# Kernel optimization log

Hardware: AMD Instinct MI355X
Metric: run time of the kernel (lower is better)

The kernel has to match this reference:

```python
import jax, jax.numpy as jnp
import numpy as np

NUM_CLASSES = 22
SKIP = 20            # skip_pixels: stride over flattened pixel index
N_STEPS = 200        # discretized steps along each voting ray
STEP = 4.0           # pixels per ray step
INLIER_T = 0.9       # inlier_threshold on direction dot-product
LABEL_T = 500.0      # label_threshold: min #pixels of a class to be valid


def _hough_forward(label_2d, vertex_pred, extents, poses, meta_data):
    B, H, W = label_2d.shape
    C = NUM_CLASSES
    HW = H * W

    # ---- strided pixel sampling (skip_pixels) ----
    idx = jnp.arange(0, HW, SKIP)                      # [P]
    P = idx.shape[0]
    ys = (idx // W).astype(jnp.float32)                # [P]
    xs = (idx % W).astype(jnp.float32)
    labels = label_2d.reshape(B, HW)[:, idx].astype(jnp.int32)   # [B,P]
    vp = vertex_pred.reshape(B, HW, C, 3)[:, idx]                # [B,P,C,3]
    # pick each pixel's predicted (dx,dy,z) for its own class label
    sel = jnp.take_along_axis(
        vp, jnp.broadcast_to(labels[:, :, None, None], (B, P, 1, 3)), axis=2
    )[:, :, 0]                                                   # [B,P,3]
    d = sel[..., :2]
    dn = d / (jnp.linalg.norm(d, axis=-1, keepdims=True) + 1e-9)  # unit dir [B,P,2]
    z = sel[..., 2]                                               # [B,P]
    fg = labels > 0                                               # foreground mask

    # ---- ray voting into per-class Hough accumulator ----
    t = (jnp.arange(N_STEPS, dtype=jnp.float32) + 1.0) * STEP     # [T]
    cx = xs[None, :, None] + dn[..., 0:1] * t[None, None, :]      # [B,P,T]
    cy = ys[None, :, None] + dn[..., 1:2] * t[None, None, :]
    cxi = jnp.round(cx).astype(jnp.int32)
    cyi = jnp.round(cy).astype(jnp.int32)
    inb = (cxi >= 0) & (cxi < W) & (cyi >= 0) & (cyi < H) & fg[..., None]
    cxi = jnp.clip(cxi, 0, W - 1)
    cyi = jnp.clip(cyi, 0, H - 1)
    bidx = jnp.arange(B, dtype=jnp.int32)[:, None, None]
    flat = ((bidx * C + labels[:, :, None]) * H + cyi) * W + cxi  # [B,P,T]
    hough = jnp.zeros((B * C * HW,), jnp.float32)
    hough = hough.at[flat.reshape(-1)].add(inb.reshape(-1).astype(jnp.float32))
    hough = hough.reshape(B, C, H, W)

    # ---- per-class peak ----
    hflat = hough.reshape(B, C, HW)
    vmax = hflat.max(-1)                               # [B,C]
    pk = jnp.argmax(hflat, axis=-1).astype(jnp.int32)  # [B,C]
    pky = (pk // W).astype(jnp.float32)
    pkx = (pk % W).astype(jnp.float32)

    # ---- validity: enough labeled pixels for the class ----
    b2 = jnp.arange(B, dtype=jnp.int32)[:, None]
    counts = jnp.zeros((B, C), jnp.float32).at[
        jnp.broadcast_to(b2, (B, HW)).reshape(-1),
        label_2d.reshape(-1).astype(jnp.int32),
    ].add(1.0)                                          # [B,C] full-res pixel counts
    cls_ids = jnp.arange(C, dtype=jnp.float32)
    valid = (counts >= LABEL_T) & (cls_ids[None, :] > 0)  # [B,C]

    # ---- inlier selection + inlier-averaged depth ----
    cx_c = jnp.take_along_axis(pkx, labels, axis=1)    # [B,P] peak of pixel's class
    cy_c = jnp.take_along_axis(pky, labels, axis=1)
    dvec = jnp.stack([cx_c - xs[None, :], cy_c - ys[None, :]], axis=-1)
    dvec = dvec / (jnp.linalg.norm(dvec, axis=-1, keepdims=True) + 1e-9)
    dot = jnp.sum(dn * dvec, axis=-1)                  # [B,P]
    inl = (fg & (dot > INLIER_T)).astype(jnp.float32)  # [B,P]
    bP = jnp.broadcast_to(b2, (B, P)).reshape(-1)
    z_sum = jnp.zeros((B, C), jnp.float32).at[bP, labels.reshape(-1)].add((z * inl).reshape(-1))
    n_inl = jnp.zeros((B, C), jnp.float32).at[bP, labels.reshape(-1)].add(inl.reshape(-1))
    depth = z_sum / jnp.maximum(n_inl, 1.0)            # [B,C]
    z_safe = jnp.where(jnp.abs(depth) > 1e-3, depth, 1.0)

    # ---- bbox from extents + intrinsics ----
    fx = meta_data[:, 0:1]                             # [B,1]
    fy = meta_data[:, 4:5]
    diam = jnp.linalg.norm(extents, axis=-1)[None, :]  # [1,C]
    half_w = 0.5 * diam * fx / z_safe
    half_h = 0.5 * diam * fy / z_safe
    vmask = valid.astype(jnp.float32)
    rois = jnp.stack([
        jnp.broadcast_to(b2.astype(jnp.float32), (B, C)),
        jnp.broadcast_to(cls_ids[None, :], (B, C)),
        pkx - half_w, pky - half_h, pkx + half_w, pky + half_h,
        vmax,
    ], axis=-1) * vmask[..., None]                     # [B,C,7]

    # ---- pose init: identity quaternion + backprojected translation ----
    Kinv = meta_data[:, 9:18].reshape(B, 3, 3)
    hom = jnp.stack([pkx, pky, jnp.ones_like(pkx)], axis=-1)      # [B,C,3]
    ray = jnp.einsum('bij,bcj->bci', Kinv, hom)
    T = depth[..., None] * ray                                    # [B,C,3]
    quat = jnp.broadcast_to(jnp.array([1.0, 0.0, 0.0, 0.0], jnp.float32), (B, C, 4))
    pose_out = jnp.concatenate([quat, T], axis=-1) * vmask[..., None]  # [B,C,7]

    return jnp.concatenate([rois, pose_out], axis=-1)  # [B,C,14]


def setup_inputs() -> dict:
    key = jax.random.key(0)
    k1, k2, k3 = jax.random.split(key, 3)
    B, H, W = 2, 480, 640
    label_2d = jax.random.randint(k1, (B, H, W), 0, NUM_CLASSES, dtype=jnp.int32)
    vertex_pred = jax.random.normal(k2, (B, H, W, 3 * NUM_CLASSES), dtype=jnp.float32)
    extents = jax.random.uniform(k3, (NUM_CLASSES, 3), minval=0.05, maxval=0.3, dtype=jnp.float32)
    poses = jnp.zeros((B, 13), jnp.float32)
    K = np.array([[1066.778, 0, 312.9869], [0, 1067.487, 241.3109], [0, 0, 1]], dtype=np.float32)
    Kinv = np.linalg.pinv(K).astype(np.float32)
    md = np.zeros((B, 48), np.float32)
    md[:, 0:9] = K.flatten()
    md[:, 9:18] = Kinv.flatten()
    meta_data = jnp.asarray(md)
    return {"label_2d": label_2d, "vertex_pred": vertex_pred, "extents": extents,
            "poses": poses, "meta_data": meta_data}


def reference(label_2d, vertex_pred, extents, poses, meta_data):
    return _hough_forward(label_2d, vertex_pred, extents, poses, meta_data)
```

## Files before the change

kernel.cpp:

```cpp
#include <hip/hip_runtime.h>
#include <math.h>

#define C_      22
#define SKIP_   20
#define NSTEP_  200
#define STEP_   4.0f
#define INL_T_  0.9f
#define LAB_T_  500
#define B_      2
#define H_      480
#define W_      640
#define HW_     (H_ * W_)
#define P_      (HW_ / SKIP_)
#define NPTS_   (B_ * P_)

#define TS_       64
#define TILES_X_  (W_ / TS_)
#define NTILES_Y_ 8
#define NTILES_   (TILES_X_ * NTILES_Y_)
#define NPLANES_  (B_ * (C_ - 1))
#define NPT_      (NPLANES_ * NTILES_)

#define CMP_BLOCKS_   (NPTS_ / 256)
#define HIST_BLOCKS_  ((B_ * HW_) / (256 * 4))

#define KEY_INIT_ 0x00000000FFFFFFFFull

__global__ __launch_bounds__(256) void compact_hist_kernel(const int* __restrict__ label,
                                                           const float* __restrict__ vp,
                                                           unsigned int* __restrict__ cls_cnt,
                                                           uint4* __restrict__ cls,
                                                           int* __restrict__ counts,
                                                           unsigned long long* __restrict__ key) {
    const int tid = threadIdx.x;
    if (blockIdx.x < CMP_BLOCKS_) {
        __shared__ int hcnt[NPLANES_];
        __shared__ int hbase[NPLANES_];
        for (int i = tid; i < NPLANES_; i += 256) hcnt[i] = 0;
        __syncthreads();
        int g   = blockIdx.x * 256 + tid;
        int b   = g / P_;
        int pi  = g - b * P_;
        int idx = pi * SKIP_;
        int lab = label[b * HW_ + idx];
        int p = -1, slot = 0;
        uint4 r;
        if (lab > 0) {
            int xi = idx % W_, yi = idx / W_;
            const float* s = vp + ((size_t)(b * HW_ + idx) * (C_ * 3)) + lab * 3;
            float dx = s[0], dy = s[1], z = s[2];
            float nrm = sqrtf(__fadd_rn(__fmul_rn(dx, dx), __fmul_rn(dy, dy))) + 1e-9f;
            float dnx = dx / nrm, dny = dy / nrm;
            p = b * (C_ - 1) + (lab - 1);
            r.x = (unsigned)xi | ((unsigned)yi << 16);
            r.y = __float_as_uint(z);
            r.z = __float_as_uint(dnx);
            r.w = __float_as_uint(dny);
            slot = atomicAdd(&hcnt[p], 1);
        }
        __syncthreads();
        for (int i = tid; i < NPLANES_; i += 256) {
            int v = hcnt[i];
            hbase[i] = v ? (int)atomicAdd(&cls_cnt[i], (unsigned)v) : 0;
        }
        __syncthreads();
        if (p >= 0)
            cls[(size_t)p * P_ + hbase[p] + slot] = r;
    } else {
        __shared__ int h[C_];
        int cb  = blockIdx.x - CMP_BLOCKS_;
        if (cb == 0 && tid < B_ * C_)
            key[tid] = KEY_INIT_;
        const int bpb = HW_ / 1024;
        int b   = cb / bpb;
        int off = (cb % bpb) * 1024 + tid * 4;
        if (tid < C_) h[tid] = 0;
        __syncthreads();
        int4 l4 = *(const int4*)(label + b * HW_ + off);
        atomicAdd(&h[l4.x], 1);
        atomicAdd(&h[l4.y], 1);
        atomicAdd(&h[l4.z], 1);
        atomicAdd(&h[l4.w], 1);
        __syncthreads();
        if (tid < C_) {
            int v = h[tid];
            if (v) atomicAdd(&counts[b * C_ + tid], v);
        }
    }
}

__global__ __launch_bounds__(256) void raster_argmax_kernel(const uint4* __restrict__ cls,
                                                            const unsigned int* __restrict__ cls_cnt,
                                                            unsigned long long* __restrict__ key) {
    __shared__ unsigned int tile[TS_ * TS_ / 2];
    __shared__ unsigned int sv[4];
    __shared__ int          si[4];
    const int tid = threadIdx.x;
    int pt = blockIdx.x;
    int p  = pt / NTILES_;
    int tl = pt % NTILES_;
    int b = p / (C_ - 1);
    int c = p % (C_ - 1) + 1;
    int x0 = (tl % TILES_X_) * TS_;
    int y0 = (tl / TILES_X_) * TS_;
    {
        uint4* t4 = (uint4*)tile;
        t4[tid]       = make_uint4(0u, 0u, 0u, 0u);
        t4[tid + 256] = make_uint4(0u, 0u, 0u, 0u);
    }
    __syncthreads();

    int m = (int)cls_cnt[p];
    if (m > P_) m = P_;
    const uint4* cl = cls + (size_t)p * P_;
    const float lox = (float)x0 - 0.51f, hix = (float)x0 + 63.51f;
    const float loy = (float)y0 - 0.51f, hiy = (float)y0 + 63.51f;
    for (int rI = tid; rI < m; rI += 256) {
        uint4 rec = cl[rI];
        float xs  = (float)(rec.x & 0xFFFFu);
        float ys  = (float)(rec.x >> 16);
        float dnx = __uint_as_float(rec.z);
        float dny = __uint_as_float(rec.w);
        float tLo = STEP_, tHi = (float)NSTEP_ * STEP_;
        bool empty = false;
        if (fabsf(dnx) > 1e-8f) {
            float ta = (lox - xs) / dnx, tb = (hix - xs) / dnx;
            float t1 = fminf(ta, tb), t2 = fmaxf(ta, tb);
            tLo = fmaxf(tLo, t1); tHi = fminf(tHi, t2);
        } else if (xs < lox || xs > hix) { empty = true; }
        if (fabsf(dny) > 1e-8f) {
            float ta = (loy - ys) / dny, tb = (hiy - ys) / dny;
            float t1 = fminf(ta, tb), t2 = fmaxf(ta, tb);
            tLo = fmaxf(tLo, t1); tHi = fminf(tHi, t2);
        } else if (ys < loy || ys > hiy) { empty = true; }
        if (empty || tLo > tHi) continue;
        int iB = (int)floorf(tLo * 0.25f) - 2; if (iB < 0) iB = 0;
        int iE = (int)ceilf(tHi * 0.25f) + 2;  if (iE > NSTEP_ - 1) iE = NSTEP_ - 1;
        for (int i = iB; i <= iE; ++i) {
            float t = (float)(i + 1) * STEP_;
            float cx = __fadd_rn(xs, __fmul_rn(dnx, t));
            float cy = __fadd_rn(ys, __fmul_rn(dny, t));
            float cxr = rintf(cx);
            float cyr = rintf(cy);
            if (cxr >= 0.0f && cxr <= (float)(W_ - 1) && cyr >= 0.0f && cyr <= (float)(H_ - 1)) {
                int lx = (int)cxr - x0;
                int ly = (int)cyr - y0;
                if ((unsigned)lx < TS_ && (unsigned)ly < TS_) {
                    int cell = ly * TS_ + lx;
                    atomicAdd(&tile[cell >> 1], 1u << ((cell & 1) * 16));
                }
            }
        }
    }
    __syncthreads();
    unsigned bv = 0u; int bi = 0;
    {
        unsigned w0 = tile[tid];
        bv = w0 & 0xFFFFu; bi = tid * 2;
        unsigned hi = w0 >> 16;
        if (hi > bv) { bv = hi; bi = tid * 2 + 1; }
    }
    #pragma unroll
    for (int j = 1; j < 8; ++j) {
        int ix = tid + j * 256;
        unsigned w = tile[ix];
        unsigned lo = w & 0xFFFFu, hi = w >> 16;
        if (lo > bv) { bv = lo; bi = ix * 2; }
        if (hi > bv) { bv = hi; bi = ix * 2 + 1; }
    }
    #pragma unroll
    for (int s = 1; s < 64; s <<= 1) {
        unsigned ov = (unsigned)__shfl_xor((int)bv, s);
        int      oi = __shfl_xor(bi, s);
        if (ov > bv || (ov == bv && oi < bi)) { bv = ov; bi = oi; }
    }
    if ((tid & 63) == 0) { sv[tid >> 6] = bv; si[tid >> 6] = bi; }
    __syncthreads();
    if (tid == 0) {
        unsigned fbv = sv[0]; int fbi = si[0];
        #pragma unroll
        for (int w = 1; w < 4; ++w) {
            unsigned ov = sv[w]; int oi = si[w];
            if (ov > fbv || (ov == fbv && oi < fbi)) { fbv = ov; fbi = oi; }
        }
        if (fbv > 0u) {
            int ly = fbi >> 6, lx = fbi & 63;
            unsigned gidx = (unsigned)((y0 + ly) * W_ + (x0 + lx));
            unsigned long long k = ((unsigned long long)fbv << 32)
                                 | (unsigned long long)(0xFFFFFFFFu - gidx);
            atomicMax(&key[b * C_ + c], k);
        }
    }
}

__global__ __launch_bounds__(256) void inlier_finalize_kernel(const uint4* __restrict__ cls,
                                                              const unsigned int* __restrict__ cls_cnt,
                                                              const unsigned long long* __restrict__ key,
                                                              float* __restrict__ z_sum,
                                                              float* __restrict__ n_inl,
                                                              int* __restrict__ counts,
                                                              const float* __restrict__ extents,
                                                              const float* __restrict__ meta,
                                                              unsigned int* __restrict__ done,
                                                              float* __restrict__ out) {
    __shared__ float zp[4];
    __shared__ float np[4];
    __shared__ int last_flag;
    const int tid = threadIdx.x;
    int p = blockIdx.x;
    int b = p / (C_ - 1);
    int c = p % (C_ - 1) + 1;
    int t_ = b * C_ + c;
    unsigned long long kp = key[t_];
    int pkv = (int)(0xFFFFFFFFu - (unsigned int)(kp & 0xFFFFFFFFull));
    float pkx = (float)(pkv % W_), pky = (float)(pkv / W_);
    int m = (int)cls_cnt[p];
    if (m > P_) m = P_;
    const uint4* cl = cls + (size_t)p * P_;
    float zacc = 0.0f, nacc = 0.0f;
    for (int r = tid; r < m; r += 256) {
        uint4 rec = cl[r];
        float xs  = (float)(rec.x & 0xFFFFu);
        float ys  = (float)(rec.x >> 16);
        float z   = __uint_as_float(rec.y);
        float dnx = __uint_as_float(rec.z);
        float dny = __uint_as_float(rec.w);
        float dvx = __fsub_rn(pkx, xs), dvy = __fsub_rn(pky, ys);
        float nrm2 = sqrtf(__fadd_rn(__fmul_rn(dvx, dvx), __fmul_rn(dvy, dvy))) + 1e-9f;
        dvx /= nrm2; dvy /= nrm2;
        float dot = __fadd_rn(__fmul_rn(dnx, dvx), __fmul_rn(dny, dvy));
        if (dot > INL_T_) { zacc += z; nacc += 1.0f; }
    }
    #pragma unroll
    for (int s = 1; s < 64; s <<= 1) {
        zacc += __shfl_xor(zacc, s);
        nacc += __shfl_xor(nacc, s);
    }
    if ((tid & 63) == 0) { zp[tid >> 6] = zacc; np[tid >> 6] = nacc; }
    __syncthreads();
    if (tid == 0) {
        z_sum[t_] = zp[0] + zp[1] + zp[2] + zp[3];
        n_inl[t_] = np[0] + np[1] + np[2] + np[3];
        __threadfence();
        unsigned prev = atomicAdd(done, 1u);
        last_flag = (prev == (unsigned)(NPLANES_ - 1)) ? 1 : 0;
    }
    __syncthreads();
    if (!last_flag) return;
    __threadfence();
    int t = tid;
    if (t >= B_ * C_) return;
    int bb = t / C_, c2 = t % C_;
    float* o = out + t * 14;
    int   cnt_t  = atomicAdd(&counts[t], 0);
    bool valid = (cnt_t >= LAB_T_) && (c2 > 0);
    if (!valid) {
        #pragma unroll
        for (int k2 = 0; k2 < 14; ++k2) o[k2] = 0.0f;
        return;
    }
    float zsum_t = atomicAdd(&z_sum[t], 0.0f);
    float ninl_t = atomicAdd(&n_inl[t], 0.0f);
    unsigned long long k = atomicAdd((unsigned long long*)&key[0] + t, 0ull);
    float depth = zsum_t / fmaxf(ninl_t, 1.0f);
    float z_safe = (fabsf(depth) > 0.001f) ? depth : 1.0f;
    float fx = meta[bb * 48 + 0];
    float fy = meta[bb * 48 + 4];
    const float* e = extents + c2 * 3;
    float diam = sqrtf(e[0]*e[0] + e[1]*e[1] + e[2]*e[2]);
    float vmax = (float)(unsigned int)(k >> 32);
    int pkv2 = (int)(0xFFFFFFFFu - (unsigned int)(k & 0xFFFFFFFFull));
    float pkx2 = (float)(pkv2 % W_), pky2 = (float)(pkv2 / W_);
    float half_w = ((0.5f * diam) * fx) / z_safe;
    float half_h = ((0.5f * diam) * fy) / z_safe;
    o[0] = (float)bb;
    o[1] = (float)c2;
    o[2] = pkx2 - half_w;
    o[3] = pky2 - half_h;
    o[4] = pkx2 + half_w;
    o[5] = pky2 + half_h;
    o[6] = vmax;
    const float* Ki = meta + bb * 48 + 9;
    float rx = Ki[0]*pkx2 + Ki[1]*pky2 + Ki[2];
    float ry = Ki[3]*pkx2 + Ki[4]*pky2 + Ki[5];
    float rz = Ki[6]*pkx2 + Ki[7]*pky2 + Ki[8];
    o[7]  = 1.0f;
    o[8]  = 0.0f;
    o[9]  = 0.0f;
    o[10] = 0.0f;
    o[11] = depth * rx;
    o[12] = depth * ry;
    o[13] = depth * rz;
}

extern "C" void kernel_launch(void* const* d_in, const int* in_sizes, int n_in,
                              void* d_out, int out_size, void* d_ws, size_t ws_size,
                              hipStream_t stream) {
    const int*   label   = (const int*)d_in[0];
    const float* vp      = (const float*)d_in[1];
    const float* extents = (const float*)d_in[2];
    const float* meta    = (const float*)d_in[4];
    float* out = (float*)d_out;

    char* ws = (char*)d_ws;
    size_t off = 0;
    unsigned int* cls_cnt = (unsigned int*)(ws + off); off += NPLANES_ * sizeof(unsigned int);
    int*          counts  = (int*)(ws + off);          off += B_ * C_ * sizeof(int);
    unsigned int* done    = (unsigned int*)(ws + off); off += sizeof(unsigned int);
    size_t zero_bytes = off;
    off = (off + 15) & ~(size_t)15;
    float* z_sum  = (float*)(ws + off); off += B_ * C_ * sizeof(float);
    float* n_inl  = (float*)(ws + off); off += B_ * C_ * sizeof(float);
    off = (off + 15) & ~(size_t)15;
    unsigned long long* key = (unsigned long long*)(ws + off);
    off += B_ * C_ * sizeof(unsigned long long);
    off = (off + 15) & ~(size_t)15;
    uint4* cls = (uint4*)(ws + off);
    off += (size_t)NPLANES_ * P_ * sizeof(uint4);

    hipMemsetAsync(d_ws, 0, zero_bytes, stream);

    compact_hist_kernel<<<CMP_BLOCKS_ + HIST_BLOCKS_, 256, 0, stream>>>(
        label, vp, cls_cnt, cls, counts, key);
    raster_argmax_kernel<<<NPT_, 256, 0, stream>>>(cls, cls_cnt, key);
    inlier_finalize_kernel<<<NPLANES_, 256, 0, stream>>>(
        cls, cls_cnt, key, z_sum, n_inl, counts, extents, meta, done, out);
}
```

Baseline: 257.6 us.

## Fuse finalize into raster kernel, use per-block directory instead of global atomics

The pipeline drops from a memset plus three launches to two kernels. The first kernel now writes records block-locally, sorted by class through an LDS prefix scan. It saves a per-block directory of start and count for each class and per-block label histogram partials, so it needs no global atomics. The raster kernel rebuilds each plane's record list by scanning the directory and binary-searching per record. The last tile block of each plane then runs the inlier reduction and writes the output, which adds scan and search overhead to every tile block.

```diff
diff --git a/kernel.cpp b/kernel.cpp
--- a/kernel.cpp
+++ b/kernel.cpp
@@ -21,80 +21,106 @@
 #define NPLANES_  (B_ * (C_ - 1))
 #define NPT_      (NPLANES_ * NTILES_)
 
-#define CMP_BLOCKS_   (NPTS_ / 256)
-#define HIST_BLOCKS_  ((B_ * HW_) / (256 * 4))
+#define K1_BLOCKS_   (NPTS_ / 256)
+#define SLAB_        (B_ * HW_ / K1_BLOCKS_)
+#define HB_PER_IMG_  (K1_BLOCKS_ / B_)
 
 #define KEY_INIT_ 0x00000000FFFFFFFFull
 
 __global__ __launch_bounds__(256) void compact_hist_kernel(const int* __restrict__ label,
                                                            const float* __restrict__ vp,
-                                                           unsigned int* __restrict__ cls_cnt,
                                                            uint4* __restrict__ cls,
-                                                           int* __restrict__ counts,
-                                                           unsigned long long* __restrict__ key) {
+                                                           unsigned int* __restrict__ dir,
+                                                           unsigned int* __restrict__ partials,
+                                                           unsigned int* __restrict__ pdone,
+                                                           unsigned long long* __restrict__ key,
+                                                           float* __restrict__ out) {
+    __shared__ int   hcnt[NPLANES_];
+    __shared__ int   hstart[NPLANES_];
+    __shared__ uint4 stage[256];
+    __shared__ int   hh[C_];
     const int tid = threadIdx.x;
-    if (blockIdx.x < CMP_BLOCKS_) {
-        __shared__ int hcnt[NPLANES_];
-        __shared__ int hbase[NPLANES_];
-        for (int i = tid; i < NPLANES_; i += 256) hcnt[i] = 0;
-        __syncthreads();
-        int g   = blockIdx.x * 256 + tid;
-        int b   = g / P_;
-        int pi  = g - b * P_;
-        int idx = pi * SKIP_;
-        int lab = label[b * HW_ + idx];
-        int p = -1, slot = 0;
-        uint4 r;
-        if (lab > 0) {
-            int xi = idx % W_, yi = idx / W_;
-            const float* s = vp + ((size_t)(b * HW_ + idx) * (C_ * 3)) + lab * 3;
-            float dx = s[0], dy = s[1], z = s[2];
-            float nrm = sqrtf(__fadd_rn(__fmul_rn(dx, dx), __fmul_rn(dy, dy))) + 1e-9f;
-            float dnx = dx / nrm, dny = dy / nrm;
-            p = b * (C_ - 1) + (lab - 1);
-            r.x = (unsigned)xi | ((unsigned)yi << 16);
-            r.y = __float_as_uint(z);
-            r.z = __float_as_uint(dnx);
-            r.w = __float_as_uint(dny);
-            slot = atomicAdd(&hcnt[p], 1);
-        }
-        __syncthreads();
-        for (int i = tid; i < NPLANES_; i += 256) {
-            int v = hcnt[i];
-            hbase[i] = v ? (int)atomicAdd(&cls_cnt[i], (unsigned)v) : 0;
-        }
-        __syncthreads();
-        if (p >= 0)
-            cls[(size_t)p * P_ + hbase[p] + slot] = r;
-    } else {
-        __shared__ int h[C_];
-        int cb  = blockIdx.x - CMP_BLOCKS_;
-        if (cb == 0 && tid < B_ * C_)
-            key[tid] = KEY_INIT_;
-        const int bpb = HW_ / 1024;
-        int b   = cb / bpb;
-        int off = (cb % bpb) * 1024 + tid * 4;
-        if (tid < C_) h[tid] = 0;
-        __syncthreads();
-        int4 l4 = *(const int4*)(label + b * HW_ + off);
-        atomicAdd(&h[l4.x], 1);
-        atomicAdd(&h[l4.y], 1);
-        atomicAdd(&h[l4.z], 1);
-        atomicAdd(&h[l4.w], 1);
-        __syncthreads();
-        if (tid < C_) {
-            int v = h[tid];
-            if (v) atomicAdd(&counts[b * C_ + tid], v);
-        }
-    }
+    const int bk  = blockIdx.x;
+
+    if (bk == 0) {
+        if (tid < B_ * C_) key[tid] = KEY_INIT_;
+        if (tid >= 64 && tid < 64 + NPLANES_) pdone[tid - 64] = 0u;
+        if (tid >= 128 && tid < 128 + 14) out[tid - 128] = 0.0f;
+        if (tid >= 160 && tid < 160 + 14) out[C_ * 14 + (tid - 160)] = 0.0f;
+    }
+
+    for (int i = tid; i < NPLANES_; i += 256) hcnt[i] = 0;
+    __syncthreads();
+    int g   = bk * 256 + tid;
+    int b   = g / P_;
+    int pi  = g - b * P_;
+    int idx = pi * SKIP_;
+    int lab = label[b * HW_ + idx];
+    int p = -1, myrank = 0;
+    uint4 r;
+    if (lab > 0) {
+        int xi = idx % W_, yi = idx / W_;
+        const float* s = vp + ((size_t)(b * HW_ + idx) * (C_ * 3)) + lab * 3;
+        float dx = s[0], dy = s[1], z = s[2];
+        float nrm = sqrtf(__fadd_rn(__fmul_rn(dx, dx), __fmul_rn(dy, dy))) + 1e-9f;
+        float dnx = dx / nrm, dny = dy / nrm;
+        p = b * (C_ - 1) + (lab - 1);
+        r.x = (unsigned)xi | ((unsigned)yi << 16);
+        r.y = __float_as_uint(z);
+        r.z = __float_as_uint(dnx);
+        r.w = __float_as_uint(dny);
+        myrank = atomicAdd(&hcnt[p], 1);
+    }
+    __syncthreads();
+    if (tid < 64) {
+        int v = (tid < NPLANES_) ? hcnt[tid] : 0;
+        int orig = v;
+        #pragma unroll
+        for (int s = 1; s < 64; s <<= 1) {
+            int u = __shfl_up(v, s);
+            if (tid >= s) v += u;
+        }
+        if (tid < NPLANES_) hstart[tid] = v - orig;
+    }
+    __syncthreads();
+    if (p >= 0) stage[hstart[p] + myrank] = r;
+    __syncthreads();
+    cls[bk * 256 + tid] = stage[tid];
+    if (tid < NPLANES_)
+        dir[bk * NPLANES_ + tid] = ((unsigned)hstart[tid] << 16) | (unsigned)hcnt[tid];
+
+    if (tid < C_) hh[tid] = 0;
+    __syncthreads();
+    const int base = bk * SLAB_;
+    #pragma unroll
+    for (int rnd = 0; rnd < SLAB_ / 1024; ++rnd) {
+        int4 l4 = *(const int4*)(label + base + rnd * 1024 + tid * 4);
+        atomicAdd(&hh[l4.x], 1);
+        atomicAdd(&hh[l4.y], 1);
+        atomicAdd(&hh[l4.z], 1);
+        atomicAdd(&hh[l4.w], 1);
+    }
+    __syncthreads();
+    if (tid < C_) partials[bk * C_ + tid] = (unsigned)hh[tid];
 }
 
-__global__ __launch_bounds__(256) void raster_argmax_kernel(const uint4* __restrict__ cls,
-                                                            const unsigned int* __restrict__ cls_cnt,
-                                                            unsigned long long* __restrict__ key) {
+__global__ __launch_bounds__(256) void raster_argmax_finalize_kernel(
+        const uint4* __restrict__ cls, const unsigned int* __restrict__ dir,
+        unsigned long long* __restrict__ key, unsigned int* __restrict__ pdone,
+        const unsigned int* __restrict__ partials,
+        const float* __restrict__ extents, const float* __restrict__ meta,
+        float* __restrict__ out) {
     __shared__ unsigned int tile[TS_ * TS_ / 2];
+    __shared__ int ebase[128];
+    __shared__ int scnt[128];
+    __shared__ int gst[128];
     __shared__ unsigned int sv[4];
     __shared__ int          si[4];
+    __shared__ float zp[4];
+    __shared__ float np[4];
+    __shared__ int last_flag;
+    __shared__ int Msh;
+    __shared__ unsigned long long kbro;
     const int tid = threadIdx.x;
     int pt = blockIdx.x;
     int p  = pt / NTILES_;
@@ -103,20 +129,41 @@
     int c = p % (C_ - 1) + 1;
     int x0 = (tl % TILES_X_) * TS_;
     int y0 = (tl / TILES_X_) * TS_;
+
     {
         uint4* t4 = (uint4*)tile;
         t4[tid]       = make_uint4(0u, 0u, 0u, 0u);
         t4[tid + 256] = make_uint4(0u, 0u, 0u, 0u);
     }
-    __syncthreads();
-
-    int m = (int)cls_cnt[p];
-    if (m > P_) m = P_;
-    const uint4* cl = cls + (size_t)p * P_;
+    if (tid < 128) {
+        int cnt = 0, st = 0;
+        if (tid < K1_BLOCKS_) {
+            unsigned w = dir[tid * NPLANES_ + p];
+            cnt = (int)(w & 0xFFFFu);
+            st  = tid * 256 + (int)(w >> 16);
+        }
+        scnt[tid] = cnt; gst[tid] = st; ebase[tid] = cnt;
+    }
+    __syncthreads();
+    for (int s = 1; s < 128; s <<= 1) {
+        int v = 0;
+        if (tid < 128) { v = ebase[tid]; if (tid >= s) v += ebase[tid - s]; }
+        __syncthreads();
+        if (tid < 128) ebase[tid] = v;
+        __syncthreads();
+    }
+    if (tid == 0) Msh = ebase[127];
+    __syncthreads();
+    if (tid < 128) ebase[tid] -= scnt[tid];
+    __syncthreads();
+    const int M = Msh;
+
     const float lox = (float)x0 - 0.51f, hix = (float)x0 + 63.51f;
     const float loy = (float)y0 - 0.51f, hiy = (float)y0 + 63.51f;
-    for (int rI = tid; rI < m; rI += 256) {
-        uint4 rec = cl[rI];
+    for (int rI = tid; rI < M; rI += 256) {
+        int lo = 0, hi = K1_BLOCKS_ - 1;
+        while (lo < hi) { int mid = (lo + hi + 1) >> 1; if (ebase[mid] <= rI) lo = mid; else hi = mid - 1; }
+        uint4 rec = cls[gst[lo] + (rI - ebase[lo])];
         float xs  = (float)(rec.x & 0xFFFFu);
         float ys  = (float)(rec.x >> 16);
         float dnx = __uint_as_float(rec.z);
@@ -157,16 +204,16 @@
     {
         unsigned w0 = tile[tid];
         bv = w0 & 0xFFFFu; bi = tid * 2;
-        unsigned hi = w0 >> 16;
-        if (hi > bv) { bv = hi; bi = tid * 2 + 1; }
+        unsigned hi2 = w0 >> 16;
+        if (hi2 > bv) { bv = hi2; bi = tid * 2 + 1; }
     }
     #pragma unroll
     for (int j = 1; j < 8; ++j) {
         int ix = tid + j * 256;
         unsigned w = tile[ix];
-        unsigned lo = w & 0xFFFFu, hi = w >> 16;
-        if (lo > bv) { bv = lo; bi = ix * 2; }
-        if (hi > bv) { bv = hi; bi = ix * 2 + 1; }
+        unsigned lo2 = w & 0xFFFFu, hi2 = w >> 16;
+        if (lo2 > bv) { bv = lo2; bi = ix * 2; }
+        if (hi2 > bv) { bv = hi2; bi = ix * 2 + 1; }
     }
     #pragma unroll
     for (int s = 1; s < 64; s <<= 1) {
@@ -191,35 +238,26 @@
             atomicMax(&key[b * C_ + c], k);
         }
     }
-}
-
-__global__ __launch_bounds__(256) void inlier_finalize_kernel(const uint4* __restrict__ cls,
-                                                              const unsigned int* __restrict__ cls_cnt,
-                                                              const unsigned long long* __restrict__ key,
-                                                              float* __restrict__ z_sum,
-                                                              float* __restrict__ n_inl,
-                                                              int* __restrict__ counts,
-                                                              const float* __restrict__ extents,
-                                                              const float* __restrict__ meta,
-                                                              unsigned int* __restrict__ done,
-                                                              float* __restrict__ out) {
-    __shared__ float zp[4];
-    __shared__ float np[4];
-    __shared__ int last_flag;
-    const int tid = threadIdx.x;
-    int p = blockIdx.x;
-    int b = p / (C_ - 1);
-    int c = p % (C_ - 1) + 1;
-    int t_ = b * C_ + c;
-    unsigned long long kp = key[t_];
-    int pkv = (int)(0xFFFFFFFFu - (unsigned int)(kp & 0xFFFFFFFFull));
+
+    if (tid == 0) {
+        __threadfence();
+        unsigned prev = atomicAdd(&pdone[p], 1u);
+        last_flag = (prev == (unsigned)(NTILES_ - 1)) ? 1 : 0;
+    }
+    __syncthreads();
+    if (!last_flag) return;
+    __threadfence();
+    if (tid == 0) kbro = atomicAdd(&key[b * C_ + c], 0ull);
+    __syncthreads();
+    unsigned long long k = kbro;
+    int pkv = (int)(0xFFFFFFFFu - (unsigned int)(k & 0xFFFFFFFFull));
     float pkx = (float)(pkv % W_), pky = (float)(pkv / W_);
-    int m = (int)cls_cnt[p];
-    if (m > P_) m = P_;
-    const uint4* cl = cls + (size_t)p * P_;
+
     float zacc = 0.0f, nacc = 0.0f;
-    for (int r = tid; r < m; r += 256) {
-        uint4 rec = cl[r];
+    for (int rI = tid; rI < M; rI += 256) {
+        int lo = 0, hi = K1_BLOCKS_ - 1;
+        while (lo < hi) { int mid = (lo + hi + 1) >> 1; if (ebase[mid] <= rI) lo = mid; else hi = mid - 1; }
+        uint4 rec = cls[gst[lo] + (rI - ebase[lo])];
         float xs  = (float)(rec.x & 0xFFFFu);
         float ys  = (float)(rec.x >> 16);
         float z   = __uint_as_float(rec.y);
@@ -238,52 +276,39 @@
     }
     if ((tid & 63) == 0) { zp[tid >> 6] = zacc; np[tid >> 6] = nacc; }
     __syncthreads();
-    if (tid == 0) {
-        z_sum[t_] = zp[0] + zp[1] + zp[2] + zp[3];
-        n_inl[t_] = np[0] + np[1] + np[2] + np[3];
-        __threadfence();
-        unsigned prev = atomicAdd(done, 1u);
-        last_flag = (prev == (unsigned)(NPLANES_ - 1)) ? 1 : 0;
-    }
-    __syncthreads();
-    if (!last_flag) return;
-    __threadfence();
-    int t = tid;
-    if (t >= B_ * C_) return;
-    int bb = t / C_, c2 = t % C_;
-    float* o = out + t * 14;
-    int   cnt_t  = atomicAdd(&counts[t], 0);
-    bool valid = (cnt_t >= LAB_T_) && (c2 > 0);
-    if (!valid) {
+    if (tid >= 64) return;
+    int cs = (tid < HB_PER_IMG_) ? (int)partials[(b * HB_PER_IMG_ + tid) * C_ + c] : 0;
+    #pragma unroll
+    for (int s = 1; s < 64; s <<= 1) cs += __shfl_xor(cs, s);
+    if (tid != 0) return;
+    float zsum_t = zp[0] + zp[1] + zp[2] + zp[3];
+    float ninl_t = np[0] + np[1] + np[2] + np[3];
+    float* o = out + (b * C_ + c) * 14;
+    if (cs < LAB_T_) {
         #pragma unroll
         for (int k2 = 0; k2 < 14; ++k2) o[k2] = 0.0f;
         return;
     }
-    float zsum_t = atomicAdd(&z_sum[t], 0.0f);
-    float ninl_t = atomicAdd(&n_inl[t], 0.0f);
-    unsigned long long k = atomicAdd((unsigned long long*)&key[0] + t, 0ull);
     float depth = zsum_t / fmaxf(ninl_t, 1.0f);
     float z_safe = (fabsf(depth) > 0.001f) ? depth : 1.0f;
-    float fx = meta[bb * 48 + 0];
-    float fy = meta[bb * 48 + 4];
-    const float* e = extents + c2 * 3;
+    float fx = meta[b * 48 + 0];
+    float fy = meta[b * 48 + 4];
+    const float* e = extents + c * 3;
     float diam = sqrtf(e[0]*e[0] + e[1]*e[1] + e[2]*e[2]);
     float vmax = (float)(unsigned int)(k >> 32);
-    int pkv2 = (int)(0xFFFFFFFFu - (unsigned int)(k & 0xFFFFFFFFull));
-    float pkx2 = (float)(pkv2 % W_), pky2 = (float)(pkv2 / W_);
     float half_w = ((0.5f * diam) * fx) / z_safe;
     float half_h = ((0.5f * diam) * fy) / z_safe;
-    o[0] = (float)bb;
-    o[1] = (float)c2;
-    o[2] = pkx2 - half_w;
-    o[3] = pky2 - half_h;
-    o[4] = pkx2 + half_w;
-    o[5] = pky2 + half_h;
+    o[0] = (float)b;
+    o[1] = (float)c;
+    o[2] = pkx - half_w;
+    o[3] = pky - half_h;
+    o[4] = pkx + half_w;
+    o[5] = pky + half_h;
     o[6] = vmax;
-    const float* Ki = meta + bb * 48 + 9;
-    float rx = Ki[0]*pkx2 + Ki[1]*pky2 + Ki[2];
-    float ry = Ki[3]*pkx2 + Ki[4]*pky2 + Ki[5];
-    float rz = Ki[6]*pkx2 + Ki[7]*pky2 + Ki[8];
+    const float* Ki = meta + b * 48 + 9;
+    float rx = Ki[0]*pkx + Ki[1]*pky + Ki[2];
+    float ry = Ki[3]*pkx + Ki[4]*pky + Ki[5];
+    float rz = Ki[6]*pkx + Ki[7]*pky + Ki[8];
     o[7]  = 1.0f;
     o[8]  = 0.0f;
     o[9]  = 0.0f;
@@ -304,25 +329,18 @@
 
     char* ws = (char*)d_ws;
     size_t off = 0;
-    unsigned int* cls_cnt = (unsigned int*)(ws + off); off += NPLANES_ * sizeof(unsigned int);
-    int*          counts  = (int*)(ws + off);          off += B_ * C_ * sizeof(int);
-    unsigned int* done    = (unsigned int*)(ws + off); off += sizeof(unsigned int);
-    size_t zero_bytes = off;
-    off = (off + 15) & ~(size_t)15;
-    float* z_sum  = (float*)(ws + off); off += B_ * C_ * sizeof(float);
-    float* n_inl  = (float*)(ws + off); off += B_ * C_ * sizeof(float);
-    off = (off + 15) & ~(size_t)15;
+    uint4* cls = (uint4*)(ws + off);
+    off += (size_t)NPTS_ * sizeof(uint4);
+    unsigned int* dir      = (unsigned int*)(ws + off); off += K1_BLOCKS_ * NPLANES_ * sizeof(unsigned int);
+    unsigned int* partials = (unsigned int*)(ws + off); off += K1_BLOCKS_ * C_ * sizeof(unsigned int);
+    unsigned int* pdone    = (unsigned int*)(ws + off); off += NPLANES_ * sizeof(unsigned int);
+    off = (off + 7) & ~(size_t)7;
     unsigned long long* key = (unsigned long long*)(ws + off);
     off += B_ * C_ * sizeof(unsigned long long);
-    off = (off + 15) & ~(size_t)15;
-    uint4* cls = (uint4*)(ws + off);
-    off += (size_t)NPLANES_ * P_ * sizeof(uint4);
-
-    hipMemsetAsync(d_ws, 0, zero_bytes, stream);
-
-    compact_hist_kernel<<<CMP_BLOCKS_ + HIST_BLOCKS_, 256, 0, stream>>>(
-        label, vp, cls_cnt, cls, counts, key);
-    raster_argmax_kernel<<<NPT_, 256, 0, stream>>>(cls, cls_cnt, key);
-    inlier_finalize_kernel<<<NPLANES_, 256, 0, stream>>>(
-        cls, cls_cnt, key, z_sum, n_inl, counts, extents, meta, done, out);
+
+
+    compact_hist_kernel<<<K1_BLOCKS_, 256, 0, stream>>>(
+        label, vp, cls, dir, partials, pdone, key, out);
+    raster_argmax_finalize_kernel<<<NPT_, 256, 0, stream>>>(
+        cls, dir, key, pdone, partials, extents, meta, out);
 }
```

After: 297.7 us. 15.6% more time.
